# Kernel tuning notes

Measured on AMD Instinct MI355X. Metric: run time of the kernel, lower is better.

## Reference

```python
import jax, jax.numpy as jnp
import numpy as np

N_NODES = 100000
N_EDGES = 1600000
F_IN = 128
N_GRAPHS = 1000
NUM_CLASSES = 2


def setup_inputs() -> dict:
    key = jax.random.key(0)
    ks = jax.random.split(key, 12)
    x = jax.random.normal(ks[0], (N_NODES, F_IN), jnp.float32)
    edge_index = jax.random.randint(ks[1], (2, N_EDGES), 0, N_NODES, dtype=jnp.int32)
    edge_weight = jnp.ones((N_EDGES,), jnp.float32)
    node_graph_index = jnp.sort(
        jax.random.randint(ks[2], (N_NODES,), 0, N_GRAPHS, dtype=jnp.int32))
    s = 0.05
    params = {
        'W0': jax.random.normal(ks[3], (F_IN, 64), jnp.float32) * s,
        'b0': jnp.zeros((64,), jnp.float32),
        'W1': jax.random.normal(ks[4], (64, 32), jnp.float32) * s,
        'b1': jnp.zeros((32,), jnp.float32),
        'Wm1': jax.random.normal(ks[5], (32, 128), jnp.float32) * s,
        'bm1': jnp.zeros((128,), jnp.float32),
        'Wm2': jax.random.normal(ks[6], (128, NUM_CLASSES), jnp.float32) * s,
        'bm2': jnp.zeros((NUM_CLASSES,), jnp.float32),
    }
    return dict(x=x, edge_index=edge_index, edge_weight=edge_weight,
                node_graph_index=node_graph_index, **params)


def _gcn_norm(edge_index, edge_weight, n_nodes):
    # renormalization trick: add self-loops, D^-1/2 (A+I) D^-1/2
    loop = jnp.arange(n_nodes, dtype=edge_index.dtype)
    src = jnp.concatenate([edge_index[0], loop])
    dst = jnp.concatenate([edge_index[1], loop])
    w = jnp.concatenate([edge_weight, jnp.ones((n_nodes,), edge_weight.dtype)])
    deg = jax.ops.segment_sum(w, dst, num_segments=n_nodes)
    dinv = jnp.where(deg > 0, jax.lax.rsqrt(jnp.maximum(deg, 1e-12)), 0.0)
    norm_w = dinv[src] * w * dinv[dst]
    return src, dst, norm_w


def _gcn_layer(h, src, dst, norm_w, W, b, n_nodes):
    m = h @ W                                # [N, out] dense transform first
    msg = m[src] * norm_w[:, None]           # [E+N, out] irregular gather
    agg = jax.ops.segment_sum(msg, dst, num_segments=n_nodes)
    return jax.nn.relu(agg + b)


def reference(x, edge_index, edge_weight, node_graph_index,
              W0, b0, W1, b1, Wm1, bm1, Wm2, bm2):
    n_nodes = x.shape[0]
    src, dst, norm_w = _gcn_norm(edge_index, edge_weight, n_nodes)
    h = _gcn_layer(x, src, dst, norm_w, W0, b0, n_nodes)   # GCN 64 + relu
    # dropout is identity at inference (training=False default)
    h = _gcn_layer(h, src, dst, norm_w, W1, b1, n_nodes)   # GCN 32 + relu
    g = jax.ops.segment_sum(h, node_graph_index, num_segments=N_GRAPHS)  # sum_pool
    g = jax.nn.relu(g @ Wm1 + bm1)
    logits = g @ Wm2 + bm2
    return logits
```

## Files before the change

### kernel.cpp

```cpp
#include <hip/hip_runtime.h>
#include <hip/hip_bf16.h>

#define F_IN 128
#define NPB 256
#define NPB_SH 8
#define MAXB 512
#define CHUNK 4096
#define CAPB 40
#define CAP 5120

typedef __attribute__((ext_vector_type(8))) short short8;
typedef __attribute__((ext_vector_type(4))) float f32x4;


__device__ __forceinline__ float bf2f(unsigned short u) {
    return __uint_as_float(((unsigned int)u) << 16);
}
__device__ __forceinline__ unsigned short f2bf(float f) {
    unsigned int x = __float_as_uint(f);
    x += 0x7FFFu + ((x >> 16) & 1u);
    return (unsigned short)(x >> 16);
}
__device__ __forceinline__ void bf8_fma(float w, uint4 r, float* a) {
    a[0] = fmaf(w, __uint_as_float(r.x << 16), a[0]);
    a[1] = fmaf(w, __uint_as_float(r.x & 0xFFFF0000u), a[1]);
    a[2] = fmaf(w, __uint_as_float(r.y << 16), a[2]);
    a[3] = fmaf(w, __uint_as_float(r.y & 0xFFFF0000u), a[3]);
    a[4] = fmaf(w, __uint_as_float(r.z << 16), a[4]);
    a[5] = fmaf(w, __uint_as_float(r.z & 0xFFFF0000u), a[5]);
    a[6] = fmaf(w, __uint_as_float(r.w << 16), a[6]);
    a[7] = fmaf(w, __uint_as_float(r.w & 0xFFFF0000u), a[7]);
}
__device__ __forceinline__ void fadd_global(float* p, float v) {
    unsafeAtomicAdd(p, v);
}

__global__ __launch_bounds__(256) void prep_w_kernel(
    const float* __restrict__ W0, const float* __restrict__ W1,
    unsigned short* __restrict__ W0t, unsigned short* __restrict__ W1t,
    float* __restrict__ Gbuf, int gtot) {
    int t = blockIdx.x * 256 + threadIdx.x;
    int stride = gridDim.x * 256;
    for (int o = t; o < 64 * 128; o += stride) {
        int n = o >> 7, k = o & 127;
        W0t[o] = f2bf(W0[k * 64 + n]);
    }
    for (int o = t; o < 32 * 64; o += stride) {
        int n = o >> 6, k = o & 63;
        W1t[o] = f2bf(W1[k * 32 + n]);
    }
    for (int o = t; o < gtot; o += stride) Gbuf[o] = 0.f;
}

__global__ __launch_bounds__(1024) void bucket_cell_kernel(
    const int* __restrict__ src, const int* __restrict__ dst,
    const float* __restrict__ ew, int* __restrict__ cntkb,
    int2* __restrict__ tmp, int E, int nbucket, int nblk) {
    __shared__ int hist[MAXB];
    const int tid = threadIdx.x;
    const int k = blockIdx.x;
    const int e0 = k * CHUNK;
    const int e1 = min(e0 + CHUNK, E);
    for (int b = tid; b < nbucket; b += 1024) hist[b] = 0;
    __syncthreads();
    const size_t reg = (size_t)k * nbucket * CAPB;
    const int e = e0 + (tid << 2);
    if (e + 4 <= e1) {
        int4 d4 = *(const int4*)(dst + e);
        int4 s4 = *(const int4*)(src + e);
        float4 w4 = *(const float4*)(ew + e);
        {
            int d = d4.x, b = d >> NPB_SH;
            int r = atomicAdd(&hist[b], 1);
            if (r < CAPB) tmp[reg + (size_t)b * CAPB + r] =
                make_int2(s4.x | ((d & (NPB - 1)) << 17), __float_as_int(w4.x));
        }
        {
            int d = d4.y, b = d >> NPB_SH;
            int r = atomicAdd(&hist[b], 1);
            if (r < CAPB) tmp[reg + (size_t)b * CAPB + r] =
                make_int2(s4.y | ((d & (NPB - 1)) << 17), __float_as_int(w4.y));
        }
        {
            int d = d4.z, b = d >> NPB_SH;
            int r = atomicAdd(&hist[b], 1);
            if (r < CAPB) tmp[reg + (size_t)b * CAPB + r] =
                make_int2(s4.z | ((d & (NPB - 1)) << 17), __float_as_int(w4.z));
        }
        {
            int d = d4.w, b = d >> NPB_SH;
            int r = atomicAdd(&hist[b], 1);
            if (r < CAPB) tmp[reg + (size_t)b * CAPB + r] =
                make_int2(s4.w | ((d & (NPB - 1)) << 17), __float_as_int(w4.w));
        }
    } else {
        for (int j = e; j < e1; ++j) {
            int d = dst[j];
            int b = d >> NPB_SH;
            int r = atomicAdd(&hist[b], 1);
            if (r < CAPB) tmp[reg + (size_t)b * CAPB + r] =
                make_int2(src[j] | ((d & (NPB - 1)) << 17), __float_as_int(ew[j]));
        }
    }
    __syncthreads();
    for (int b = tid; b < nbucket; b += 1024)
        cntkb[(size_t)b * nblk + k] = min(hist[b], CAPB);
}

__global__ __launch_bounds__(1024) void csr_kernel(
    const int2* __restrict__ tmp, const int* __restrict__ cntkb,
    int2* __restrict__ es, int* __restrict__ rstart, int* __restrict__ rend,
    float* __restrict__ dinv, int N, int nbucket, int nblk) {
    __shared__ int cnt[256];
    __shared__ float dw[256];
    __shared__ int off[256];
    __shared__ int cur[256];
    const int t = threadIdx.x;
    const int b = blockIdx.x;
    const int n0 = b << NPB_SH;
    const size_t seg = (size_t)b * CAP;
    if (t < 256) {
        cnt[t] = 0;
        dw[t] = 0.f;
    }
    __syncthreads();
    for (int k = t; k < nblk; k += 1024) {
        const int cc = cntkb[(size_t)b * nblk + k];
        const int2* cp = tmp + ((size_t)k * nbucket + b) * CAPB;
#pragma unroll 2
        for (int j = 0; j < cc; ++j) {
            int2 e2 = cp[j];
            int d = e2.x >> 17;
            atomicAdd(&cnt[d], 1);
            atomicAdd(&dw[d], __int_as_float(e2.y));
        }
    }
    __syncthreads();
    if (t < 256) off[t] = cnt[t];
    __syncthreads();
    for (int o = 1; o < 256; o <<= 1) {
        int x = 0;
        if (t >= o && t < 256) x = off[t - o];
        __syncthreads();
        if (t < 256) off[t] += x;
        __syncthreads();
    }
    if (t < 256) {
        int v = cnt[t];
        int excl = off[t] - v;
        cur[t] = excl;
        int n = n0 + t;
        if (n < N) {
            rstart[n] = (int)seg + excl;
            rend[n] = (int)seg + excl + v;
            dinv[n] = rsqrtf(fmaxf(1.f + dw[t], 1e-12f));
        }
    }
    __syncthreads();
    for (int k = t; k < nblk; k += 1024) {
        const int cc = cntkb[(size_t)b * nblk + k];
        const int2* cp = tmp + ((size_t)k * nbucket + b) * CAPB;
#pragma unroll 2
        for (int j = 0; j < cc; ++j) {
            int2 e2 = cp[j];
            int d = e2.x >> 17;
            int r = atomicAdd(&cur[d], 1);
            es[seg + r] = make_int2(e2.x & 0x1FFFF, e2.y);
        }
    }
}

__global__ __launch_bounds__(256) void gemm1_mfma_kernel(
    const float* __restrict__ X, const unsigned short* __restrict__ W0t,
    const float* __restrict__ dinv, unsigned short* __restrict__ M, int N) {
    __shared__ unsigned short Bs[64][136];
    const int tid = threadIdx.x;
    for (int i = tid; i < 64 * 32; i += 256) {
        int n = i >> 5, k4 = i & 31;
        ushort4 v = ((const ushort4*)W0t)[i];
        *(ushort4*)&Bs[n][k4 * 4] = v;
    }
    __syncthreads();
    const int wave = tid >> 6, lane = tid & 63;
    const int m = lane & 15, q = lane >> 4;
    const int rowA = blockIdx.x * 64 + wave * 16 + m;
    const bool rok = rowA < N;
    const float* xrow = X + (size_t)rowA * 128;
    f32x4 acc[4] = {};
#pragma unroll
    for (int ks = 0; ks < 4; ++ks) {
        int k0 = ks * 32 + q * 8;
        float4 u0 = make_float4(0.f, 0.f, 0.f, 0.f);
        float4 u1 = make_float4(0.f, 0.f, 0.f, 0.f);
        if (rok) {
            u0 = *(const float4*)(xrow + k0);
            u1 = *(const float4*)(xrow + k0 + 4);
        }
        short8 a;
        a[0] = (short)f2bf(u0.x); a[1] = (short)f2bf(u0.y);
        a[2] = (short)f2bf(u0.z); a[3] = (short)f2bf(u0.w);
        a[4] = (short)f2bf(u1.x); a[5] = (short)f2bf(u1.y);
        a[6] = (short)f2bf(u1.z); a[7] = (short)f2bf(u1.w);
#pragma unroll
        for (int ct = 0; ct < 4; ++ct) {
            short8 b = *(const short8*)&Bs[ct * 16 + m][k0];
            acc[ct] = __builtin_amdgcn_mfma_f32_16x16x32_bf16(a, b, acc[ct], 0, 0, 0);
        }
    }
#pragma unroll
    for (int r = 0; r < 4; ++r) {
        int crow = blockIdx.x * 64 + wave * 16 + q * 4 + r;
        if (crow < N) {
            float d = dinv[crow];
#pragma unroll
            for (int ct = 0; ct < 4; ++ct)
                M[(size_t)crow * 64 + ct * 16 + m] = f2bf(acc[ct][r] * d);
        }
    }
}

__global__ __launch_bounds__(256) void gemm2_mfma_kernel(
    const unsigned short* __restrict__ H1, const unsigned short* __restrict__ W1t,
    const float* __restrict__ dinv, unsigned short* __restrict__ M, int N) {
    __shared__ unsigned short Bs[32][72];
    const int tid = threadIdx.x;
    for (int i = tid; i < 32 * 16; i += 256) {
        int n = i >> 4, k4 = i & 15;
        ushort4 v = ((const ushort4*)W1t)[i];
        *(ushort4*)&Bs[n][k4 * 4] = v;
    }
    __syncthreads();
    const int wave = tid >> 6, lane = tid & 63;
    const int m = lane & 15, q = lane >> 4;
    const int rowA = blockIdx.x * 64 + wave * 16 + m;
    const bool rok = rowA < N;
    const short8 az = {0, 0, 0, 0, 0, 0, 0, 0};
    f32x4 acc[2] = {};
#pragma unroll
    for (int ks = 0; ks < 2; ++ks) {
        int k0 = ks * 32 + q * 8;
        short8 a = rok ? *(const short8*)(H1 + (size_t)rowA * 64 + k0) : az;
#pragma unroll
        for (int ct = 0; ct < 2; ++ct) {
            short8 b = *(const short8*)&Bs[ct * 16 + m][k0];
            acc[ct] = __builtin_amdgcn_mfma_f32_16x16x32_bf16(a, b, acc[ct], 0, 0, 0);
        }
    }
#pragma unroll
    for (int r = 0; r < 4; ++r) {
        int crow = blockIdx.x * 64 + wave * 16 + q * 4 + r;
        if (crow < N) {
            float d = dinv[crow];
#pragma unroll
            for (int ct = 0; ct < 2; ++ct)
                M[(size_t)crow * 32 + ct * 16 + m] = f2bf(acc[ct][r] * d);
        }
    }
}

__global__ __launch_bounds__(256) void pull1_kernel(
    const int* __restrict__ rstart, const int* __restrict__ rend,
    const int2* __restrict__ es, const unsigned short* __restrict__ M,
    const float* __restrict__ dinv, const float* __restrict__ bias,
    unsigned short* __restrict__ H1, int N) {
    const int lane = threadIdx.x & 63;
    const int wave = threadIdx.x >> 6;
    const int nd = lane >> 5;
    const int node = blockIdx.x * 8 + wave * 2 + nd;
    if (node >= N) return;
    const int c = lane & 7;
    const int q = (lane >> 3) & 3;
    float acc[8] = {0.f, 0.f, 0.f, 0.f, 0.f, 0.f, 0.f, 0.f};
    if (q == 0) {
        uint4 r = *(const uint4*)(M + (size_t)node * 64 + c * 8);
        bf8_fma(1.f, r, acc);
    }
    const int b = rstart[node], e = rend[node];
    const int len = e - b;
    const int base = len >> 2, rem = len & 3;
    int p = b + q * base + min(q, rem);
    const int pe = p + base + (q < rem ? 1 : 0);
    for (; p + 2 <= pe; p += 2) {
        int4 v = *(const int4*)(es + p);
        uint4 r0 = *(const uint4*)(M + (size_t)v.x * 64 + c * 8);
        uint4 r1 = *(const uint4*)(M + (size_t)v.z * 64 + c * 8);
        bf8_fma(__int_as_float(v.y), r0, acc);
        bf8_fma(__int_as_float(v.w), r1, acc);
    }
    if (p < pe) {
        int2 ed = es[p];
        uint4 r = *(const uint4*)(M + (size_t)ed.x * 64 + c * 8);
        bf8_fma(__int_as_float(ed.y), r, acc);
    }
#pragma unroll
    for (int off = 8; off <= 16; off <<= 1)
#pragma unroll
        for (int k = 0; k < 8; ++k) acc[k] += __shfl_xor(acc[k], off);
    if (q == 0) {
        float d = dinv[node];
        const float* bp = bias + c * 8;
        float4 b0v = *(const float4*)(bp);
        float4 b1v = *(const float4*)(bp + 4);
        unsigned short o[8];
        o[0] = f2bf(fmaxf(fmaf(d, acc[0], b0v.x), 0.f));
        o[1] = f2bf(fmaxf(fmaf(d, acc[1], b0v.y), 0.f));
        o[2] = f2bf(fmaxf(fmaf(d, acc[2], b0v.z), 0.f));
        o[3] = f2bf(fmaxf(fmaf(d, acc[3], b0v.w), 0.f));
        o[4] = f2bf(fmaxf(fmaf(d, acc[4], b1v.x), 0.f));
        o[5] = f2bf(fmaxf(fmaf(d, acc[5], b1v.y), 0.f));
        o[6] = f2bf(fmaxf(fmaf(d, acc[6], b1v.z), 0.f));
        o[7] = f2bf(fmaxf(fmaf(d, acc[7], b1v.w), 0.f));
        uint4 pk;
        pk.x = (unsigned int)o[0] | ((unsigned int)o[1] << 16);
        pk.y = (unsigned int)o[2] | ((unsigned int)o[3] << 16);
        pk.z = (unsigned int)o[4] | ((unsigned int)o[5] << 16);
        pk.w = (unsigned int)o[6] | ((unsigned int)o[7] << 16);
        *(uint4*)(H1 + (size_t)node * 64 + c * 8) = pk;
    }
}

__global__ __launch_bounds__(256) void pull2_pool_kernel(
    const int* __restrict__ rstart, const int* __restrict__ rend,
    const int2* __restrict__ es, const unsigned short* __restrict__ M,
    const float* __restrict__ dinv, const float* __restrict__ bias,
    const int* __restrict__ ngi, float* __restrict__ g, int N) {
    __shared__ float4 sh[16][8];
    __shared__ int sgx[16];
    const int t = threadIdx.x;
    const int lane = t & 63;
    const int nl = t >> 4;
    const int node = blockIdx.x * 16 + nl;
    const int c = lane & 3;
    const int q = (lane >> 2) & 3;
    const bool valid = node < N;
    float acc[8] = {0.f, 0.f, 0.f, 0.f, 0.f, 0.f, 0.f, 0.f};
    if (valid) {
        if (q == 0) {
            uint4 r = *(const uint4*)(M + (size_t)node * 32 + c * 8);
            bf8_fma(1.f, r, acc);
        }
        const int b = rstart[node], e = rend[node];
        const int len = e - b;
        const int base = len >> 2, rem = len & 3;
        int p = b + q * base + min(q, rem);
        const int pe = p + base + (q < rem ? 1 : 0);
        for (; p + 2 <= pe; p += 2) {
            int4 v = *(const int4*)(es + p);
            uint4 r0 = *(const uint4*)(M + (size_t)v.x * 32 + c * 8);
            uint4 r1 = *(const uint4*)(M + (size_t)v.z * 32 + c * 8);
            bf8_fma(__int_as_float(v.y), r0, acc);
            bf8_fma(__int_as_float(v.w), r1, acc);
        }
        if (p < pe) {
            int2 ed = es[p];
            uint4 r = *(const uint4*)(M + (size_t)ed.x * 32 + c * 8);
            bf8_fma(__int_as_float(ed.y), r, acc);
        }
#pragma unroll
        for (int off = 4; off <= 8; off <<= 1)
#pragma unroll
            for (int k = 0; k < 8; ++k) acc[k] += __shfl_xor(acc[k], off);
    }
    if (q == 0) {
        float4 o0 = make_float4(0.f, 0.f, 0.f, 0.f);
        float4 o1 = make_float4(0.f, 0.f, 0.f, 0.f);
        if (valid) {
            float d = dinv[node];
            const float* bp = bias + c * 8;
            float4 b0v = *(const float4*)(bp);
            float4 b1v = *(const float4*)(bp + 4);
            o0.x = fmaxf(fmaf(d, acc[0], b0v.x), 0.f);
            o0.y = fmaxf(fmaf(d, acc[1], b0v.y), 0.f);
            o0.z = fmaxf(fmaf(d, acc[2], b0v.z), 0.f);
            o0.w = fmaxf(fmaf(d, acc[3], b0v.w), 0.f);
            o1.x = fmaxf(fmaf(d, acc[4], b1v.x), 0.f);
            o1.y = fmaxf(fmaf(d, acc[5], b1v.y), 0.f);
            o1.z = fmaxf(fmaf(d, acc[6], b1v.z), 0.f);
            o1.w = fmaxf(fmaf(d, acc[7], b1v.w), 0.f);
        }
        sh[nl][c * 2] = o0;
        sh[nl][c * 2 + 1] = o1;
        if (c == 0) sgx[nl] = valid ? ngi[node] : -1;
    }
    __syncthreads();
    if (t < 8) {
        int cc = t;
        float4 a = make_float4(0.f, 0.f, 0.f, 0.f);
        int cg = -1;
        for (int i = 0; i < 16; ++i) {
            int gi = sgx[i];
            if (gi < 0) continue;
            if (gi != cg) {
                if (cg >= 0) {
                    float* gp = g + cg * 32 + cc * 4;
                    fadd_global(gp + 0, a.x); fadd_global(gp + 1, a.y);
                    fadd_global(gp + 2, a.z); fadd_global(gp + 3, a.w);
                }
                cg = gi;
                a = sh[i][cc];
            } else {
                float4 tv = sh[i][cc];
                a.x += tv.x; a.y += tv.y; a.z += tv.z; a.w += tv.w;
            }
        }
        if (cg >= 0) {
            float* gp = g + cg * 32 + cc * 4;
            fadd_global(gp + 0, a.x); fadd_global(gp + 1, a.y);
            fadd_global(gp + 2, a.z); fadd_global(gp + 3, a.w);
        }
    }
}

__global__ __launch_bounds__(128) void mlp_kernel(
    const float* __restrict__ g, const float* __restrict__ Wm1,
    const float* __restrict__ bm1, const float* __restrict__ Wm2,
    const float* __restrict__ bm2, float* __restrict__ out) {
    __shared__ float sg[32];
    __shared__ float red[4];
    int b = blockIdx.x, t = threadIdx.x;
    if (t < 32) sg[t] = g[b * 32 + t];
    __syncthreads();
    float acc = bm1[t];
#pragma unroll
    for (int k = 0; k < 32; ++k) acc = fmaf(sg[k], Wm1[k * 128 + t], acc);
    float h = fmaxf(acc, 0.f);
    float p0 = h * Wm2[t * 2 + 0];
    float p1 = h * Wm2[t * 2 + 1];
#pragma unroll
    for (int off = 32; off >= 1; off >>= 1) {
        p0 += __shfl_xor(p0, off);
        p1 += __shfl_xor(p1, off);
    }
    if ((t & 63) == 0) {
        red[(t >> 6) * 2 + 0] = p0;
        red[(t >> 6) * 2 + 1] = p1;
    }
    __syncthreads();
    if (t < 2) out[b * 2 + t] = bm2[t] + red[t] + red[2 + t];
}


extern "C" void kernel_launch(void* const* d_in, const int* in_sizes, int n_in,
                              void* d_out, int out_size, void* d_ws, size_t ws_size,
                              hipStream_t stream) {
    const float* x   = (const float*)d_in[0];
    const int*   ei  = (const int*)d_in[1];
    const float* ew  = (const float*)d_in[2];
    const int*   ngi = (const int*)d_in[3];
    const float* W0  = (const float*)d_in[4];
    const float* b0  = (const float*)d_in[5];
    const float* W1  = (const float*)d_in[6];
    const float* b1  = (const float*)d_in[7];
    const float* Wm1 = (const float*)d_in[8];
    const float* bm1 = (const float*)d_in[9];
    const float* Wm2 = (const float*)d_in[10];
    const float* bm2 = (const float*)d_in[11];
    float* out = (float*)d_out;

    const int N = in_sizes[0] / F_IN;
    const int E = in_sizes[1] / 2;
    const int G = out_size / 2;
    const int* srcp = ei;
    const int* dstp = ei + E;
    const int NBUCKET = (N + NPB - 1) >> NPB_SH;
    const int NBLK = (E + CHUNK - 1) / CHUNK;

    char* wsb = (char*)d_ws;
    size_t off = 0;
    auto alloc = [&](size_t bytes) {
        char* p = wsb + off;
        off += (bytes + 255) & ~(size_t)255;
        return p;
    };
    float* dinv     = (float*)alloc((size_t)N * 4);
    int*   rstart   = (int*)  alloc((size_t)N * 4);
    int*   rend     = (int*)  alloc((size_t)N * 4);
    int*   cntkb    = (int*)  alloc((size_t)NBUCKET * NBLK * 4);
    int2*  tmp      = (int2*) alloc((size_t)NBLK * NBUCKET * CAPB * 8);
    int2*  es       = (int2*) alloc((size_t)NBUCKET * CAP * 8);
    unsigned short* W0t = (unsigned short*)alloc(64 * 128 * 2);
    unsigned short* W1t = (unsigned short*)alloc(32 * 64 * 2);
    unsigned short* M   = (unsigned short*)alloc((size_t)N * 64 * 2);
    unsigned short* H1  = (unsigned short*)alloc((size_t)N * 64 * 2);
    float* Gbuf     = (float*)alloc((size_t)G * 32 * 4);
    unsigned short* m1p = M;

    prep_w_kernel<<<8, 256, 0, stream>>>(W0, W1, W0t, W1t, Gbuf, G * 32);
    bucket_cell_kernel<<<NBLK, 1024, 0, stream>>>(srcp, dstp, ew, cntkb, tmp, E, NBUCKET, NBLK);
    csr_kernel<<<NBUCKET, 1024, 0, stream>>>(tmp, cntkb, es, rstart, rend, dinv, N, NBUCKET, NBLK);

    gemm1_mfma_kernel<<<(N + 63) / 64, 256, 0, stream>>>(x, W0t, dinv, M, N);
    pull1_kernel<<<(N + 7) / 8, 256, 0, stream>>>(rstart, rend, es, M, dinv, b0, H1, N);

    gemm2_mfma_kernel<<<(N + 63) / 64, 256, 0, stream>>>(H1, W1t, dinv, m1p, N);
    pull2_pool_kernel<<<(N + 15) / 16, 256, 0, stream>>>(rstart, rend, es, m1p, dinv, b1, ngi, Gbuf, N);

    mlp_kernel<<<G, 128, 0, stream>>>(Gbuf, Wm1, bm1, Wm2, bm2, out);
}
```

Measured before the change: 243.7 us.

## Fuse layer-2 GEMM into layer-1 aggregation and fold weight prep into bucketing

Layer-1 aggregation now computes the 64x32 transform in-block from shared memory (fp32 FMA on relu output) and writes the dinv-scaled layer-2 messages directly. This drops the H1 round trip and the separate gemm2 MFMA launch. Weight transpose and pooling-buffer zeroing move into an extra block of the bucketing kernel, removing another launch. The CSR builder now parallelises over all (chunk, slot) pairs with cached counts instead of serial per-chunk loops. The trade is that pull1 carries extra shared memory, a block barrier and scalar-FMA work, which can reduce occupancy.

```diff
diff --git a/kernel.cpp b/kernel.cpp
--- a/kernel.cpp
+++ b/kernel.cpp
@@ -35,30 +35,23 @@
     unsafeAtomicAdd(p, v);
 }
 
-__global__ __launch_bounds__(256) void prep_w_kernel(
-    const float* __restrict__ W0, const float* __restrict__ W1,
-    unsigned short* __restrict__ W0t, unsigned short* __restrict__ W1t,
-    float* __restrict__ Gbuf, int gtot) {
-    int t = blockIdx.x * 256 + threadIdx.x;
-    int stride = gridDim.x * 256;
-    for (int o = t; o < 64 * 128; o += stride) {
-        int n = o >> 7, k = o & 127;
-        W0t[o] = f2bf(W0[k * 64 + n]);
-    }
-    for (int o = t; o < 32 * 64; o += stride) {
-        int n = o >> 6, k = o & 63;
-        W1t[o] = f2bf(W1[k * 32 + n]);
-    }
-    for (int o = t; o < gtot; o += stride) Gbuf[o] = 0.f;
-}
-
-__global__ __launch_bounds__(1024) void bucket_cell_kernel(
+__global__ __launch_bounds__(1024) void bucket_prep_kernel(
     const int* __restrict__ src, const int* __restrict__ dst,
     const float* __restrict__ ew, int* __restrict__ cntkb,
-    int2* __restrict__ tmp, int E, int nbucket, int nblk) {
+    int2* __restrict__ tmp, const float* __restrict__ W0,
+    unsigned short* __restrict__ W0t, float* __restrict__ Gbuf,
+    int E, int nbucket, int nblk, int gtot) {
     __shared__ int hist[MAXB];
     const int tid = threadIdx.x;
     const int k = blockIdx.x;
+    if (k == nblk) {
+        for (int o = tid; o < 64 * 128; o += 1024) {
+            int n = o >> 7, kk = o & 127;
+            W0t[o] = f2bf(W0[kk * 64 + n]);
+        }
+        for (int o = tid; o < gtot; o += 1024) Gbuf[o] = 0.f;
+        return;
+    }
     const int e0 = k * CHUNK;
     const int e1 = min(e0 + CHUNK, E);
     for (int b = tid; b < nbucket; b += 1024) hist[b] = 0;
@@ -111,6 +104,7 @@
     const int2* __restrict__ tmp, const int* __restrict__ cntkb,
     int2* __restrict__ es, int* __restrict__ rstart, int* __restrict__ rend,
     float* __restrict__ dinv, int N, int nbucket, int nblk) {
+    __shared__ int ccs[MAXB];
     __shared__ int cnt[256];
     __shared__ float dw[256];
     __shared__ int off[256];
@@ -123,13 +117,13 @@
         cnt[t] = 0;
         dw[t] = 0.f;
     }
-    __syncthreads();
-    for (int k = t; k < nblk; k += 1024) {
-        const int cc = cntkb[(size_t)b * nblk + k];
-        const int2* cp = tmp + ((size_t)k * nbucket + b) * CAPB;
-#pragma unroll 2
-        for (int j = 0; j < cc; ++j) {
-            int2 e2 = cp[j];
+    for (int k = t; k < nblk; k += 1024) ccs[k] = cntkb[(size_t)b * nblk + k];
+    __syncthreads();
+    const int tot = nblk * CAPB;
+    for (int s = t; s < tot; s += 1024) {
+        int k = s / CAPB, j = s - k * CAPB;
+        if (j < ccs[k]) {
+            int2 e2 = tmp[((size_t)k * nbucket + b) * CAPB + j];
             int d = e2.x >> 17;
             atomicAdd(&cnt[d], 1);
             atomicAdd(&dw[d], __int_as_float(e2.y));
@@ -157,12 +151,10 @@
         }
     }
     __syncthreads();
-    for (int k = t; k < nblk; k += 1024) {
-        const int cc = cntkb[(size_t)b * nblk + k];
-        const int2* cp = tmp + ((size_t)k * nbucket + b) * CAPB;
-#pragma unroll 2
-        for (int j = 0; j < cc; ++j) {
-            int2 e2 = cp[j];
+    for (int s = t; s < tot; s += 1024) {
+        int k = s / CAPB, j = s - k * CAPB;
+        if (j < ccs[k]) {
+            int2 e2 = tmp[((size_t)k * nbucket + b) * CAPB + j];
             int d = e2.x >> 17;
             int r = atomicAdd(&cur[d], 1);
             es[seg + r] = make_int2(e2.x & 0x1FFFF, e2.y);
@@ -219,103 +211,74 @@
     }
 }
 
-__global__ __launch_bounds__(256) void gemm2_mfma_kernel(
-    const unsigned short* __restrict__ H1, const unsigned short* __restrict__ W1t,
-    const float* __restrict__ dinv, unsigned short* __restrict__ M, int N) {
-    __shared__ unsigned short Bs[32][72];
-    const int tid = threadIdx.x;
-    for (int i = tid; i < 32 * 16; i += 256) {
-        int n = i >> 4, k4 = i & 15;
-        ushort4 v = ((const ushort4*)W1t)[i];
-        *(ushort4*)&Bs[n][k4 * 4] = v;
-    }
-    __syncthreads();
-    const int wave = tid >> 6, lane = tid & 63;
-    const int m = lane & 15, q = lane >> 4;
-    const int rowA = blockIdx.x * 64 + wave * 16 + m;
-    const bool rok = rowA < N;
-    const short8 az = {0, 0, 0, 0, 0, 0, 0, 0};
-    f32x4 acc[2] = {};
-#pragma unroll
-    for (int ks = 0; ks < 2; ++ks) {
-        int k0 = ks * 32 + q * 8;
-        short8 a = rok ? *(const short8*)(H1 + (size_t)rowA * 64 + k0) : az;
-#pragma unroll
-        for (int ct = 0; ct < 2; ++ct) {
-            short8 b = *(const short8*)&Bs[ct * 16 + m][k0];
-            acc[ct] = __builtin_amdgcn_mfma_f32_16x16x32_bf16(a, b, acc[ct], 0, 0, 0);
-        }
-    }
-#pragma unroll
-    for (int r = 0; r < 4; ++r) {
-        int crow = blockIdx.x * 64 + wave * 16 + q * 4 + r;
-        if (crow < N) {
-            float d = dinv[crow];
-#pragma unroll
-            for (int ct = 0; ct < 2; ++ct)
-                M[(size_t)crow * 32 + ct * 16 + m] = f2bf(acc[ct][r] * d);
-        }
-    }
-}
-
-__global__ __launch_bounds__(256) void pull1_kernel(
+__global__ __launch_bounds__(256) void pull1_l2_kernel(
     const int* __restrict__ rstart, const int* __restrict__ rend,
     const int2* __restrict__ es, const unsigned short* __restrict__ M,
     const float* __restrict__ dinv, const float* __restrict__ bias,
-    unsigned short* __restrict__ H1, int N) {
-    const int lane = threadIdx.x & 63;
-    const int wave = threadIdx.x >> 6;
-    const int nd = lane >> 5;
-    const int node = blockIdx.x * 8 + wave * 2 + nd;
-    if (node >= N) return;
+    const float* __restrict__ W1, unsigned short* __restrict__ m1p, int N) {
+    __shared__ float w1s[64 * 32];
+    __shared__ float h1s[8 * 64];
+    __shared__ float sdv[8];
+    const int t = threadIdx.x;
+    for (int i = t; i < 64 * 32; i += 256) w1s[i] = W1[i];
+    const int lane = t & 63;
+    const int d = t >> 5;
+    const int node = blockIdx.x * 8 + d;
     const int c = lane & 7;
     const int q = (lane >> 3) & 3;
-    float acc[8] = {0.f, 0.f, 0.f, 0.f, 0.f, 0.f, 0.f, 0.f};
-    if (q == 0) {
-        uint4 r = *(const uint4*)(M + (size_t)node * 64 + c * 8);
-        bf8_fma(1.f, r, acc);
-    }
-    const int b = rstart[node], e = rend[node];
-    const int len = e - b;
-    const int base = len >> 2, rem = len & 3;
-    int p = b + q * base + min(q, rem);
-    const int pe = p + base + (q < rem ? 1 : 0);
-    for (; p + 2 <= pe; p += 2) {
-        int4 v = *(const int4*)(es + p);
-        uint4 r0 = *(const uint4*)(M + (size_t)v.x * 64 + c * 8);
-        uint4 r1 = *(const uint4*)(M + (size_t)v.z * 64 + c * 8);
-        bf8_fma(__int_as_float(v.y), r0, acc);
-        bf8_fma(__int_as_float(v.w), r1, acc);
-    }
-    if (p < pe) {
-        int2 ed = es[p];
-        uint4 r = *(const uint4*)(M + (size_t)ed.x * 64 + c * 8);
-        bf8_fma(__int_as_float(ed.y), r, acc);
-    }
-#pragma unroll
-    for (int off = 8; off <= 16; off <<= 1)
-#pragma unroll
-        for (int k = 0; k < 8; ++k) acc[k] += __shfl_xor(acc[k], off);
-    if (q == 0) {
-        float d = dinv[node];
-        const float* bp = bias + c * 8;
-        float4 b0v = *(const float4*)(bp);
-        float4 b1v = *(const float4*)(bp + 4);
-        unsigned short o[8];
-        o[0] = f2bf(fmaxf(fmaf(d, acc[0], b0v.x), 0.f));
-        o[1] = f2bf(fmaxf(fmaf(d, acc[1], b0v.y), 0.f));
-        o[2] = f2bf(fmaxf(fmaf(d, acc[2], b0v.z), 0.f));
-        o[3] = f2bf(fmaxf(fmaf(d, acc[3], b0v.w), 0.f));
-        o[4] = f2bf(fmaxf(fmaf(d, acc[4], b1v.x), 0.f));
-        o[5] = f2bf(fmaxf(fmaf(d, acc[5], b1v.y), 0.f));
-        o[6] = f2bf(fmaxf(fmaf(d, acc[6], b1v.z), 0.f));
-        o[7] = f2bf(fmaxf(fmaf(d, acc[7], b1v.w), 0.f));
-        uint4 pk;
-        pk.x = (unsigned int)o[0] | ((unsigned int)o[1] << 16);
-        pk.y = (unsigned int)o[2] | ((unsigned int)o[3] << 16);
-        pk.z = (unsigned int)o[4] | ((unsigned int)o[5] << 16);
-        pk.w = (unsigned int)o[6] | ((unsigned int)o[7] << 16);
-        *(uint4*)(H1 + (size_t)node * 64 + c * 8) = pk;
+    const bool valid = node < N;
+    if (valid) {
+        float acc[8] = {0.f, 0.f, 0.f, 0.f, 0.f, 0.f, 0.f, 0.f};
+        if (q == 0) {
+            uint4 r = *(const uint4*)(M + (size_t)node * 64 + c * 8);
+            bf8_fma(1.f, r, acc);
+        }
+        const int b = rstart[node], e = rend[node];
+        const int len = e - b;
+        const int base = len >> 2, rem = len & 3;
+        int p = b + q * base + min(q, rem);
+        const int pe = p + base + (q < rem ? 1 : 0);
+        for (; p + 2 <= pe; p += 2) {
+            int4 v = *(const int4*)(es + p);
+            uint4 r0 = *(const uint4*)(M + (size_t)v.x * 64 + c * 8);
+            uint4 r1 = *(const uint4*)(M + (size_t)v.z * 64 + c * 8);
+            bf8_fma(__int_as_float(v.y), r0, acc);
+            bf8_fma(__int_as_float(v.w), r1, acc);
+        }
+        if (p < pe) {
+            int2 ed = es[p];
+            uint4 r = *(const uint4*)(M + (size_t)ed.x * 64 + c * 8);
+            bf8_fma(__int_as_float(ed.y), r, acc);
+        }
+#pragma unroll
+        for (int off = 8; off <= 16; off <<= 1)
+#pragma unroll
+            for (int k = 0; k < 8; ++k) acc[k] += __shfl_xor(acc[k], off);
+        if (q == 0) {
+            float dv = dinv[node];
+            const float* bp = bias + c * 8;
+            float4 b0v = *(const float4*)(bp);
+            float4 b1v = *(const float4*)(bp + 4);
+            float* hp = h1s + d * 64 + c * 8;
+            hp[0] = fmaxf(fmaf(dv, acc[0], b0v.x), 0.f);
+            hp[1] = fmaxf(fmaf(dv, acc[1], b0v.y), 0.f);
+            hp[2] = fmaxf(fmaf(dv, acc[2], b0v.z), 0.f);
+            hp[3] = fmaxf(fmaf(dv, acc[3], b0v.w), 0.f);
+            hp[4] = fmaxf(fmaf(dv, acc[4], b1v.x), 0.f);
+            hp[5] = fmaxf(fmaf(dv, acc[5], b1v.y), 0.f);
+            hp[6] = fmaxf(fmaf(dv, acc[6], b1v.z), 0.f);
+            hp[7] = fmaxf(fmaf(dv, acc[7], b1v.w), 0.f);
+            if (c == 0) sdv[d] = dv;
+        }
+    }
+    __syncthreads();
+    if (valid) {
+        const int n = t & 31;
+        const float* hp = h1s + d * 64;
+        float a2 = 0.f;
+#pragma unroll
+        for (int k = 0; k < 64; ++k) a2 = fmaf(hp[k], w1s[k * 32 + n], a2);
+        m1p[(size_t)node * 32 + n] = f2bf(sdv[d] * a2);
     }
 }
 
@@ -479,21 +442,18 @@
     int2*  tmp      = (int2*) alloc((size_t)NBLK * NBUCKET * CAPB * 8);
     int2*  es       = (int2*) alloc((size_t)NBUCKET * CAP * 8);
     unsigned short* W0t = (unsigned short*)alloc(64 * 128 * 2);
-    unsigned short* W1t = (unsigned short*)alloc(32 * 64 * 2);
     unsigned short* M   = (unsigned short*)alloc((size_t)N * 64 * 2);
-    unsigned short* H1  = (unsigned short*)alloc((size_t)N * 64 * 2);
+    unsigned short* m1p = (unsigned short*)alloc((size_t)N * 32 * 2);
     float* Gbuf     = (float*)alloc((size_t)G * 32 * 4);
-    unsigned short* m1p = M;
-
-    prep_w_kernel<<<8, 256, 0, stream>>>(W0, W1, W0t, W1t, Gbuf, G * 32);
-    bucket_cell_kernel<<<NBLK, 1024, 0, stream>>>(srcp, dstp, ew, cntkb, tmp, E, NBUCKET, NBLK);
+
+    bucket_prep_kernel<<<NBLK + 1, 1024, 0, stream>>>(
+        srcp, dstp, ew, cntkb, tmp, W0, W0t, Gbuf, E, NBUCKET, NBLK, G * 32);
     csr_kernel<<<NBUCKET, 1024, 0, stream>>>(tmp, cntkb, es, rstart, rend, dinv, N, NBUCKET, NBLK);
 
     gemm1_mfma_kernel<<<(N + 63) / 64, 256, 0, stream>>>(x, W0t, dinv, M, N);
-    pull1_kernel<<<(N + 7) / 8, 256, 0, stream>>>(rstart, rend, es, M, dinv, b0, H1, N);
-
-    gemm2_mfma_kernel<<<(N + 63) / 64, 256, 0, stream>>>(H1, W1t, dinv, m1p, N);
+
+    pull1_l2_kernel<<<(N + 7) / 8, 256, 0, stream>>>(rstart, rend, es, M, dinv, b0, W1, m1p, N);
+
     pull2_pool_kernel<<<(N + 15) / 16, 256, 0, stream>>>(rstart, rend, es, m1p, dinv, b1, ngi, Gbuf, N);
-
     mlp_kernel<<<G, 128, 0, stream>>>(Gbuf, Wm1, bm1, Wm2, bm2, out);
 }
```

Result: no change. 244.6 us (+0.4%).
